# Kernel optimization log

Hardware: AMD Instinct MI355X
Metric: run time of the kernel (lower is better)

## Reference

```python
import jax, jax.numpy as jnp
import numpy as np
from jax import lax

B, C, OUT, H, W = 4, 64, 64, 128, 128
BN_EPS = 1e-5
DN = ('NCHW', 'OIHW', 'NCHW')


def conv3x3(x, w, pad=1, dil=1, groups=1):
    return lax.conv_general_dilated(
        x, w, window_strides=(1, 1), padding=[(pad, pad), (pad, pad)],
        rhs_dilation=(dil, dil), dimension_numbers=DN,
        feature_group_count=groups)


def setup_inputs() -> dict:
    key = jax.random.key(0)
    ks = jax.random.split(key, 10)
    return {
        'x': jax.random.normal(ks[0], (B, C, H, W), jnp.float32),
        'kernel': jax.random.normal(ks[1], (B, 3, OUT, C, 3, 3), jnp.float32) * 0.05,
        'conv_mask_w': jax.random.normal(ks[2], (3, C, 3, 3), jnp.float32) * 0.05,
        'conv_mask_b': jnp.zeros((3,), jnp.float32),
        'conv_out_w': jax.random.normal(ks[3], (OUT, OUT * 4, 3, 3), jnp.float32) * 0.05,
        'conv_out_b': jnp.zeros((OUT,), jnp.float32),
        'bn_gamma': jnp.ones((OUT,), jnp.float32),
        'bn_beta': jnp.zeros((OUT,), jnp.float32),
        'bn_mean': jax.random.normal(ks[4], (OUT,), jnp.float32) * 0.1,
        'bn_var': jax.random.uniform(ks[5], (OUT,), jnp.float32, 0.5, 1.5),
    }


def reference(x, kernel, conv_mask_w, conv_mask_b, conv_out_w, conv_out_b,
              bn_gamma, bn_beta, bn_mean, bn_var):
    b, c, h, w = x.shape
    out_ch = conv_out_w.shape[0]

    # mask branch: conv -> Softmax2d (softmax over channel dim)
    masks = conv3x3(x, conv_mask_w) + conv_mask_b[None, :, None, None]
    masks = jax.nn.softmax(masks, axis=1)  # [b, 3, h, w]

    # per-sample mask-weighted copies: [b, 3, c, h, w] -> grouped-conv layout
    xm = (x[:, None, :, :, :] * masks[:, :, None, :, :]).reshape(1, b * 3 * c, h, w)

    # all four branches use the SAME kernel slice kernel[:, 0:3] (as in the source)
    kw = kernel[:, 0:3].reshape(-1, c, 3, 3)  # [b*3*out, c, 3, 3]

    def branch(dil):
        y = conv3x3(xm, kw, pad=dil, dil=dil, groups=b * 3)
        return y.reshape(b, 3, out_ch, h, w).sum(axis=1)  # sum over the 3 masks

    cat = jnp.concatenate([branch(1), branch(3), branch(5), branch(7)], axis=1)

    out = conv3x3(cat, conv_out_w) + conv_out_b[None, :, None, None]
    # BatchNorm2d in eval mode (running stats)
    inv = bn_gamma / jnp.sqrt(bn_var + BN_EPS)
    out = out * inv[None, :, None, None] + (bn_beta - bn_mean * inv)[None, :, None, None]
    out = jax.nn.relu(out)
    return (out, masks)
```

## Files before the change

kernel.cpp:

```cpp
#include <hip/hip_runtime.h>
#include <math.h>

typedef __bf16 bf16;
typedef __bf16 bf16x8 __attribute__((ext_vector_type(8)));
typedef __bf16 bf16x4 __attribute__((ext_vector_type(4)));
typedef float  f32x4  __attribute__((ext_vector_type(4)));

#define HW        16384
#define OUT_ELEMS 4194304

#define XM_ROW    (142 * 64)
#define XM_PLANE  (142 * XM_ROW)
#define CAT_ROW   (130 * 256)
#define CAT_PLANE (130 * CAT_ROW)

#define LPX 72

__global__ void k_mask1(const float* __restrict__ x, const float* __restrict__ mw,
                        float* __restrict__ part) {
  int y = blockIdx.x, b = blockIdx.y, cg = blockIdx.z;
  int tx = threadIdx.x;
  float a0 = 0.f, a1 = 0.f, a2 = 0.f;
#pragma unroll
  for (int ci = 0; ci < 8; ++ci) {
    int c = cg * 8 + ci;
    const float* xp = x + ((size_t)(b * 64 + c)) * HW;
    const float* w0 = mw + (0 * 64 + c) * 9;
    const float* w1 = mw + (1 * 64 + c) * 9;
    const float* w2 = mw + (2 * 64 + c) * 9;
#pragma unroll
    for (int ky = 0; ky < 3; ++ky) {
      int yy = y + ky - 1;
      if ((unsigned)yy >= 128u) continue;
#pragma unroll
      for (int kx = 0; kx < 3; ++kx) {
        int xx = tx + kx - 1;
        if ((unsigned)xx >= 128u) continue;
        float xv = xp[yy * 128 + xx];
        a0 += xv * w0[ky * 3 + kx];
        a1 += xv * w1[ky * 3 + kx];
        a2 += xv * w2[ky * 3 + kx];
      }
    }
  }
  size_t base = (size_t)((b * 8 + cg) * 3) * HW + y * 128 + tx;
  part[base]          = a0;
  part[base + HW]     = a1;
  part[base + 2 * HW] = a2;
}

__global__ void k_xmt(const float* __restrict__ x, const float* __restrict__ part,
                      const float* __restrict__ mb, float* __restrict__ masks,
                      bf16* __restrict__ xm_p,
                      const float* __restrict__ kern, const float* __restrict__ w2,
                      bf16* __restrict__ kern_t, bf16* __restrict__ w2_t) {
  int yp = blockIdx.x;
  int m = blockIdx.y, b = blockIdx.z;
  int t = threadIdx.x;

  {
    const int NK  = 442368;
    const int NW2 = 147456;
    int bid2 = yp + 142 * (m + 3 * b);
#pragma unroll
    for (int it = 0; it < 2; ++it) {
      int idx = (bid2 + it * 1704) * 256 + t;
      if (idx < NK) {
        int j    = idx & 7;
        int lane = (idx >> 3) & 63;
        int km   = (idx >> 9) & 7;
        int tap  = (idx >> 12) % 9;
        int bm   = idx / 36864;
        int o = (km >> 1) * 16 + (lane & 15);
        int c = (km & 1) * 32 + (lane >> 4) * 8 + j;
        kern_t[idx] = (bf16)kern[(((bm * 64 + o) * 64 + c) * 9) + tap];
      } else if (idx < NK + NW2) {
        int j = idx - NK;
        int j8   = j & 7;
        int lane = (j >> 3) & 63;
        int km   = (j >> 9) & 7;
        int cq   = (j >> 12) & 3;
        int tap  = j >> 14;
        int oc = (km >> 1) * 16 + (lane & 15);
        int ch = cq * 64 + (km & 1) * 32 + (lane >> 4) * 8 + j8;
        w2_t[j] = (bf16)w2[(oc * 256 + ch) * 9 + tap];
      }
    }
  }

  bf16* prow = xm_p + (size_t)(b * 3 + m) * XM_PLANE + (size_t)yp * XM_ROW;
  bf16x8 z = {};
  if (yp < 7 || yp >= 135) {
#pragma unroll
    for (int i = 0; i < 5; ++i) {
      int u = i * 256 + t;
      if (u < 1136) ((bf16x8*)prow)[u] = z;
    }
    return;
  }
  if (t < 56) ((bf16x8*)prow)[t] = z;
  else if (t < 112) ((bf16x8*)(prow + 135 * 64))[t - 56] = z;

  int y = yp - 7;
  __shared__ float tile[64 * 130];
  __shared__ float mrow_s[128];
#pragma unroll
  for (int i = 0; i < 32; ++i) {
    int u = i * 256 + t;
    int c = u >> 7, xx = u & 127;
    tile[c * 130 + xx] = x[((size_t)(b * 64 + c)) * HW + y * 128 + xx];
  }
  if (t < 128) {
    float a0 = mb[0], a1 = mb[1], a2 = mb[2];
    int off = y * 128 + t;
#pragma unroll
    for (int cg = 0; cg < 8; ++cg) {
      size_t base = (size_t)((b * 8 + cg) * 3) * HW + off;
      a0 += part[base];
      a1 += part[base + HW];
      a2 += part[base + 2 * HW];
    }
    float mx = fmaxf(a0, fmaxf(a1, a2));
    float e0 = __expf(a0 - mx), e1 = __expf(a1 - mx), e2 = __expf(a2 - mx);
    float inv = 1.0f / (e0 + e1 + e2);
    float v0 = e0 * inv, v1 = e1 * inv, v2 = e2 * inv;
    mrow_s[t] = (m == 0) ? v0 : (m == 1) ? v1 : v2;
    if (m == 0) {
      size_t mbase = ((size_t)b * 3) * HW + off;
      masks[mbase]          = v0;
      masks[mbase + HW]     = v1;
      masks[mbase + 2 * HW] = v2;
    }
  }
  __syncthreads();
  bf16* orow = prow + 7 * 64;
#pragma unroll
  for (int i = 0; i < 4; ++i) {
    int u = i * 256 + t;
    int cg = u & 7, xx = u >> 3;
    float mv = mrow_s[xx];
    bf16x8 v;
#pragma unroll
    for (int j = 0; j < 8; ++j)
      v[j] = (bf16)(tile[(cg * 8 + j) * 130 + xx] * mv);
    *(bf16x8*)(orow + xx * 64 + cg * 8) = v;
  }
}

__global__ __launch_bounds__(256, 2) void k_branch(const bf16* __restrict__ xm_p,
                                                   const bf16* __restrict__ kern_t,
                                                   bf16* __restrict__ cat_p) {
  __shared__ bf16 sb[4][2][78 * 64];
  int bid = blockIdx.x;
  {
    int id = bid * 256 + threadIdx.x;
    if (id < 4 * 16512) {
      int plane = id / 16512, j = id % 16512;
      bf16* base = cat_p + (size_t)plane * CAT_PLANE;
      bf16x8 zv = {};
      if (j < 8320) {
        int row = (j / 4160) * 129;
        int off = (j % 4160) * 8;
        *(bf16x8*)(base + (size_t)row * CAT_ROW + off) = zv;
      } else {
        int k = j - 8320;
        int row = 1 + (k >> 6);
        int idx2 = k & 63;
        int col = (idx2 >> 5) * 129;
        int ch8 = (idx2 & 31) * 8;
        *(bf16x8*)(base + (size_t)row * CAT_ROW + col * 256 + ch8) = zv;
      }
    }
  }
  int xcd = bid & 7;
  int i   = bid >> 3;
  int b   = xcd >> 1;
  int di  = ((xcd & 1) << 1) | (i & 1);
  int ypr = i >> 1;
  int d   = 1 + 2 * di;
  int t    = threadIdx.x;
  int lane = t & 63;
  int wave = t >> 6;
  int yr   = wave >> 1;
  int wh   = wave & 1;
  int y    = ypr * 2 + yr;
  int lanelo = lane & 15;
  int quad = lane >> 4;

  const bf16* plane0 = xm_p + (size_t)(b * 3) * XM_PLANE;
  const bf16* wb0    = kern_t + (size_t)(b * 27) * 4096 + lane * 8;
  const int gp0 = wh * 64 + 7 - d;

  bf16* mysb0 = &sb[wave][0][0];
  bf16* mysb1 = &sb[wave][1][0];

  bf16x8 sreg[10];
  {
    const bf16* s0 = plane0 + (size_t)(y + 7 - d) * XM_ROW + gp0 * 64;
#pragma unroll
    for (int r = 0; r < 10; ++r) {
      int u = r * 64 + lane;
      if (u < 624) sreg[r] = *(const bf16x8*)(s0 + u * 8);
    }
#pragma unroll
    for (int r = 0; r < 10; ++r) {
      int u = r * 64 + lane;
      if (u < 624) {
        int px = u >> 3, sl = u & 7;
        *(bf16x8*)(mysb0 + px * 64 + ((sl ^ (px & 7)) << 3)) = sreg[r];
      }
    }
    const bf16* s1 = plane0 + (size_t)(y + 7) * XM_ROW + gp0 * 64;
#pragma unroll
    for (int r = 0; r < 10; ++r) {
      int u = r * 64 + lane;
      if (u < 624) sreg[r] = *(const bf16x8*)(s1 + u * 8);
    }
  }

  f32x4 acc[4][4] = {};

#pragma unroll
  for (int p = 0; p < 9; ++p) {
    int m = p / 3, ky = p % 3;
    const bf16* wtap = wb0 + (size_t)(m * 9 + ky * 3) * 4096;

    if (p < 8) {
      bf16* wbuf = ((p + 1) & 1) ? mysb1 : mysb0;
#pragma unroll
      for (int r = 0; r < 10; ++r) {
        int u = r * 64 + lane;
        if (u < 624) {
          int px = u >> 3, sl = u & 7;
          *(bf16x8*)(wbuf + px * 64 + ((sl ^ (px & 7)) << 3)) = sreg[r];
        }
      }
    }
    if (p < 7) {
      int pn = p + 2;
      int mn = pn / 3, kyn = pn % 3;
      const bf16* sn = plane0 + (size_t)mn * XM_PLANE
                     + (size_t)(y + 7 + d * (kyn - 1)) * XM_ROW + gp0 * 64;
#pragma unroll
      for (int r = 0; r < 10; ++r) {
        int u = r * 64 + lane;
        if (u < 624) sreg[r] = *(const bf16x8*)(sn + u * 8);
      }
    }
    const bf16* rbuf = (p & 1) ? mysb1 : mysb0;
#pragma unroll
    for (int kx = 0; kx < 3; ++kx) {
      bf16x8 areg[2][4];
#pragma unroll
      for (int kci = 0; kci < 2; ++kci)
#pragma unroll
        for (int mt = 0; mt < 4; ++mt)
          areg[kci][mt] = *(const bf16x8*)(wtap + kx * 4096 + (mt * 2 + kci) * 512);
      int lpx0 = lanelo + d * kx;
      int p7   = lpx0 & 7;
#pragma unroll
      for (int kci = 0; kci < 2; ++kci) {
        int swsl = ((quad + 4 * kci) ^ p7) << 3;
        bf16x8 bv[4];
#pragma unroll
        for (int nt = 0; nt < 4; ++nt)
          bv[nt] = *(const bf16x8*)(rbuf + (lpx0 + nt * 16) * 64 + swsl);
        __builtin_amdgcn_s_setprio(1);
#pragma unroll
        for (int mt = 0; mt < 4; ++mt)
#pragma unroll
          for (int nt = 0; nt < 4; ++nt)
            acc[mt][nt] = __builtin_amdgcn_mfma_f32_16x16x32_bf16(areg[kci][mt], bv[nt], acc[mt][nt], 0, 0, 0);
        __builtin_amdgcn_s_setprio(0);
      }
    }
  }

  bf16* cp = cat_p + (size_t)b * CAT_PLANE + (size_t)(y + 1) * CAT_ROW + di * 64;
#pragma unroll
  for (int mt = 0; mt < 4; ++mt) {
#pragma unroll
    for (int nt = 0; nt < 4; ++nt) {
      int px = wh * 64 + nt * 16 + lanelo;
      bf16x4 v;
#pragma unroll
      for (int r = 0; r < 4; ++r) v[r] = (bf16)acc[mt][nt][r];
      *(bf16x4*)(cp + (size_t)(px + 1) * 256 + (mt * 16 + quad * 4)) = v;
    }
  }
}

__global__ __launch_bounds__(256, 2) void k_final(const bf16* __restrict__ cat_p,
                                                  const bf16* __restrict__ w2_t,
                                                  const float* __restrict__ cb,
                                                  const float* __restrict__ gamma,
                                                  const float* __restrict__ beta,
                                                  const float* __restrict__ mean,
                                                  const float* __restrict__ var,
                                                  float* __restrict__ out) {
  __shared__ bf16 sb[4][2][66 * LPX];
  int bid = blockIdx.x;
  int xcd = bid & 7;
  int b   = xcd >> 1;
  int ypr = ((bid >> 3) << 1) | (xcd & 1);
  int t    = threadIdx.x;
  int lane = t & 63;
  int wave = t >> 6;
  int yr   = wave >> 1;
  int wh   = wave & 1;
  int y    = ypr * 2 + yr;
  int lanelo = lane & 15;
  int quad = lane >> 4;

  const bf16* cb2 = cat_p + (size_t)b * CAT_PLANE + (size_t)(wh * 64) * 256;
  const bf16* wb0 = w2_t + lane * 8;

  bf16* mysb0 = &sb[wave][0][0];
  bf16* mysb1 = &sb[wave][1][0];

  bf16x8 sreg[9];
  {
    const bf16* s0 = cb2 + (size_t)y * CAT_ROW;
#pragma unroll
    for (int r = 0; r < 9; ++r) {
      int u = r * 64 + lane;
      if (u < 528) sreg[r] = *(const bf16x8*)(s0 + (u >> 3) * 256 + (u & 7) * 8);
    }
#pragma unroll
    for (int r = 0; r < 9; ++r) {
      int u = r * 64 + lane;
      if (u < 528) *(bf16x8*)(mysb0 + (u >> 3) * LPX + (u & 7) * 8) = sreg[r];
    }
    const bf16* s1 = cb2 + (size_t)(y + 1) * CAT_ROW;
#pragma unroll
    for (int r = 0; r < 9; ++r) {
      int u = r * 64 + lane;
      if (u < 528) sreg[r] = *(const bf16x8*)(s1 + (u >> 3) * 256 + (u & 7) * 8);
    }
  }

  f32x4 acc[4][4] = {};

#pragma unroll
  for (int p = 0; p < 12; ++p) {
    int cq = p / 3, ky = p % 3;

    if (p < 11) {
      bf16* wbuf = ((p + 1) & 1) ? mysb1 : mysb0;
#pragma unroll
      for (int r = 0; r < 9; ++r) {
        int u = r * 64 + lane;
        if (u < 528) *(bf16x8*)(wbuf + (u >> 3) * LPX + (u & 7) * 8) = sreg[r];
      }
    }
    if (p < 10) {
      int pn = p + 2;
      int cqn = pn / 3, kyn = pn % 3;
      const bf16* sn = cb2 + (size_t)(y + kyn) * CAT_ROW + cqn * 64;
#pragma unroll
      for (int r = 0; r < 9; ++r) {
        int u = r * 64 + lane;
        if (u < 528) sreg[r] = *(const bf16x8*)(sn + (u >> 3) * 256 + (u & 7) * 8);
      }
    }
    const bf16* rbuf = (p & 1) ? mysb1 : mysb0;
#pragma unroll
    for (int kx = 0; kx < 3; ++kx) {
      bf16x8 areg[2][4];
      const bf16* wt = wb0 + (size_t)(((ky * 3 + kx) * 4 + cq) * 8) * 512;
#pragma unroll
      for (int kci = 0; kci < 2; ++kci)
#pragma unroll
        for (int mt = 0; mt < 4; ++mt)
          areg[kci][mt] = *(const bf16x8*)(wt + (mt * 2 + kci) * 512);
      int lpx0 = lanelo + kx;
#pragma unroll
      for (int kci = 0; kci < 2; ++kci) {
        bf16x8 bv[4];
#pragma unroll
        for (int nt = 0; nt < 4; ++nt)
          bv[nt] = *(const bf16x8*)(rbuf + (lpx0 + nt * 16) * LPX + quad * 8 + kci * 32);
        __builtin_amdgcn_s_setprio(1);
#pragma unroll
        for (int mt = 0; mt < 4; ++mt)
#pragma unroll
          for (int nt = 0; nt < 4; ++nt)
            acc[mt][nt] = __builtin_amdgcn_mfma_f32_16x16x32_bf16(areg[kci][mt], bv[nt], acc[mt][nt], 0, 0, 0);
        __builtin_amdgcn_s_setprio(0);
      }
    }
  }

#pragma unroll
  for (int mt = 0; mt < 4; ++mt) {
#pragma unroll
    for (int nt = 0; nt < 4; ++nt) {
      int px = wh * 64 + nt * 16 + lanelo;
#pragma unroll
      for (int r = 0; r < 4; ++r) {
        int oc = mt * 16 + quad * 4 + r;
        float inv = gamma[oc] * rsqrtf(var[oc] + 1e-5f);
        float v = (acc[mt][nt][r] + cb[oc]) * inv + beta[oc] - mean[oc] * inv;
        out[((size_t)(b * 64 + oc)) * HW + y * 128 + px] = fmaxf(v, 0.0f);
      }
    }
  }
}

extern "C" void kernel_launch(void* const* d_in, const int* in_sizes, int n_in,
                              void* d_out, int out_size, void* d_ws, size_t ws_size,
                              hipStream_t stream) {
  const float* x     = (const float*)d_in[0];
  const float* kern  = (const float*)d_in[1];
  const float* mw    = (const float*)d_in[2];
  const float* mb    = (const float*)d_in[3];
  const float* w2    = (const float*)d_in[4];
  const float* cb    = (const float*)d_in[5];
  const float* gamma = (const float*)d_in[6];
  const float* beta  = (const float*)d_in[7];
  const float* mean  = (const float*)d_in[8];
  const float* var   = (const float*)d_in[9];

  float* out   = (float*)d_out;
  float* masks = out + OUT_ELEMS;

  char* ws = (char*)d_ws;
  bf16* xm_p   = (bf16*)(ws);
  bf16* cat_p  = (bf16*)(ws + 30971904);
  bf16* kern_t = (bf16*)(ws + 65583104);
  bf16* w2_t   = (bf16*)(ws + 66467840);
  float* part  = (float*)(ws + 30971904);

  k_mask1<<<dim3(128, 4, 8), 128, 0, stream>>>(x, mw, part);
  k_xmt<<<dim3(142, 3, 4), 256, 0, stream>>>(x, part, mb, masks, xm_p, kern, w2, kern_t, w2_t);
  k_branch<<<1024, 256, 0, stream>>>(xm_p, kern_t, cat_p);
  k_final<<<256, 256, 0, stream>>>(cat_p, w2_t, cb, gamma, beta, mean, var, out);
}
```

Baseline: 210.3 us.

## Split final conv reduction across wave pairs and double the block count

The final 3x3 conv kernel now gives each block one output row instead of two. The two wave pairs in a block each handle half of the 256 input channels, and the second pair hands its fp32 partial accumulators to the first through shared memory before the epilogue. The grid doubles to 512 blocks, which raises parallelism and shortens each wave's serial reduction loop. The cost is an extra shared-memory round trip and a barrier, and adjacent-row reuse of cat loads within a block is lost.

Result: no change. 208.7 us (-0.8%).

```diff
diff --git a/kernel.cpp b/kernel.cpp
--- a/kernel.cpp
+++ b/kernel.cpp
@@ -302,13 +302,12 @@
   int bid = blockIdx.x;
   int xcd = bid & 7;
   int b   = xcd >> 1;
-  int ypr = ((bid >> 3) << 1) | (xcd & 1);
+  int y   = ((bid >> 3) << 1) | (xcd & 1);
   int t    = threadIdx.x;
   int lane = t & 63;
   int wave = t >> 6;
-  int yr   = wave >> 1;
   int wh   = wave & 1;
-  int y    = ypr * 2 + yr;
+  int kq   = wave >> 1;
   int lanelo = lane & 15;
   int quad = lane >> 4;
 
@@ -320,7 +319,7 @@
 
   bf16x8 sreg[9];
   {
-    const bf16* s0 = cb2 + (size_t)y * CAT_ROW;
+    const bf16* s0 = cb2 + (size_t)y * CAT_ROW + (kq * 2) * 64;
 #pragma unroll
     for (int r = 0; r < 9; ++r) {
       int u = r * 64 + lane;
@@ -331,7 +330,7 @@
       int u = r * 64 + lane;
       if (u < 528) *(bf16x8*)(mysb0 + (u >> 3) * LPX + (u & 7) * 8) = sreg[r];
     }
-    const bf16* s1 = cb2 + (size_t)(y + 1) * CAT_ROW;
+    const bf16* s1 = cb2 + (size_t)(y + 1) * CAT_ROW + (kq * 2) * 64;
 #pragma unroll
     for (int r = 0; r < 9; ++r) {
       int u = r * 64 + lane;
@@ -342,10 +341,10 @@
   f32x4 acc[4][4] = {};
 
 #pragma unroll
-  for (int p = 0; p < 12; ++p) {
-    int cq = p / 3, ky = p % 3;
-
-    if (p < 11) {
+  for (int p = 0; p < 6; ++p) {
+    int cq = kq * 2 + p / 3, ky = p % 3;
+
+    if (p < 5) {
       bf16* wbuf = ((p + 1) & 1) ? mysb1 : mysb0;
 #pragma unroll
       for (int r = 0; r < 9; ++r) {
@@ -353,9 +352,9 @@
         if (u < 528) *(bf16x8*)(wbuf + (u >> 3) * LPX + (u & 7) * 8) = sreg[r];
       }
     }
-    if (p < 10) {
+    if (p < 4) {
       int pn = p + 2;
-      int cqn = pn / 3, kyn = pn % 3;
+      int cqn = kq * 2 + pn / 3, kyn = pn % 3;
       const bf16* sn = cb2 + (size_t)(y + kyn) * CAT_ROW + cqn * 64;
 #pragma unroll
       for (int r = 0; r < 9; ++r) {
@@ -391,6 +390,22 @@
     }
   }
 
+  if (kq == 1) {
+    float* fs = (float*)mysb0;
+#pragma unroll
+    for (int mt = 0; mt < 4; ++mt)
+#pragma unroll
+      for (int nt = 0; nt < 4; ++nt)
+#pragma unroll
+        for (int r = 0; r < 4; ++r)
+          fs[((mt * 4 + nt) * 4 + r) * 64 + lane] = acc[mt][nt][r];
+  }
+  asm volatile("s_waitcnt lgkmcnt(0)" ::: "memory");
+  __builtin_amdgcn_s_barrier();
+  __builtin_amdgcn_sched_barrier(0);
+  if (kq == 1) return;
+
+  const float* pf = (const float*)&sb[wave ^ 2][0][0];
 #pragma unroll
   for (int mt = 0; mt < 4; ++mt) {
 #pragma unroll
@@ -399,8 +414,9 @@
 #pragma unroll
       for (int r = 0; r < 4; ++r) {
         int oc = mt * 16 + quad * 4 + r;
+        float s = acc[mt][nt][r] + pf[((mt * 4 + nt) * 4 + r) * 64 + lane];
         float inv = gamma[oc] * rsqrtf(var[oc] + 1e-5f);
-        float v = (acc[mt][nt][r] + cb[oc]) * inv + beta[oc] - mean[oc] * inv;
+        float v = (s + cb[oc]) * inv + beta[oc] - mean[oc] * inv;
         out[((size_t)(b * 64 + oc)) * HW + y * 128 + px] = fmaxf(v, 0.0f);
       }
     }
@@ -434,5 +450,5 @@
   k_mask1<<<dim3(128, 4, 8), 128, 0, stream>>>(x, mw, part);
   k_xmt<<<dim3(142, 3, 4), 256, 0, stream>>>(x, part, mb, masks, xm_p, kern, w2, kern_t, w2_t);
   k_branch<<<1024, 256, 0, stream>>>(xm_p, kern_t, cat_p);
-  k_final<<<256, 256, 0, stream>>>(cat_p, w2_t, cb, gamma, beta, mean, var, out);
+  k_final<<<512, 256, 0, stream>>>(cat_p, w2_t, cb, gamma, beta, mean, var, out);
 }
```
